# Performance work log

Hardware: AMD Instinct MI355X
Metric: run time of the kernel (lower is better)

The kernel has to match this reference:

```python
import jax, jax.numpy as jnp
import numpy as np

N_NODES = 50000
NEG_SLOPE = 0.2


def setup_inputs() -> dict:
    key = jax.random.key(0)
    k1, k2, k3, k4 = jax.random.split(key, 4)
    N, E, F, H, C = 50000, 800000, 128, 4, 32
    x = jax.random.normal(k1, (N, F), dtype=jnp.float32)
    edge_index = jax.random.randint(k2, (2, E), 0, N, dtype=jnp.int32)
    weight = jax.random.normal(k3, (F, H * C), dtype=jnp.float32) * 0.1  # glorot-ish scale
    att = jax.random.normal(k4, (1, H, 2 * C), dtype=jnp.float32) * 0.1
    bias = jnp.zeros((C,), dtype=jnp.float32)
    return {"x": x, "edge_index": edge_index, "weight": weight, "att": att, "bias": bias}


def reference(x, edge_index, weight, att, bias):
    N = x.shape[0]
    H, C2 = att.shape[1], att.shape[2]
    C = C2 // 2
    # linear projection -> [N, H, C]
    xw = jnp.matmul(x, weight).reshape(N, H, C)
    row, col = edge_index[0], edge_index[1]
    # per-edge attention logits: gather both endpoints, concat along channel
    x_i = xw[row]                     # [E, H, C]
    x_j = xw[col]                     # [E, H, C]
    cat_x = jnp.concatenate([x_i, x_j], axis=-1)      # [E, H, 2C]
    alpha = jnp.sum(cat_x * att, axis=-1)             # [E, H]
    alpha = jnp.where(alpha >= 0, alpha, NEG_SLOPE * alpha)  # leaky_relu
    # segment softmax grouped by row (source index, as in the torch code)
    seg_max = jax.ops.segment_max(alpha, row, num_segments=N)
    seg_max = jnp.where(jnp.isfinite(seg_max), seg_max, 0.0)
    alpha = jnp.exp(alpha - seg_max[row])
    seg_sum = jax.ops.segment_sum(alpha, row, num_segments=N)
    alpha = alpha / (seg_sum[row] + 1e-16)            # [E, H]
    # PyG propagate: message = alpha * x_j where x_j = x[edge_index[0]],
    # aggregated (scatter-add) into target = edge_index[1]
    msg = alpha[..., None] * xw[row]                  # [E, H, C]
    out = jax.ops.segment_sum(msg, col, num_segments=N)  # [N, H, C]
    out = out.mean(axis=1) + bias                     # concat=False -> head mean, + bias
    return out
```

## Files before the change

kernel.cpp:

```cpp
#include <hip/hip_runtime.h>
#include <hip/hip_fp16.h>

#define FDIM 128
#define HEADS 4
#define CD 32
#define BM 64
#define XPAD 68

static __device__ __forceinline__ unsigned short f2bf(float v) {
    unsigned u = __float_as_uint(v);
    u += 0x7FFF + ((u >> 16) & 1);
    return (unsigned short)(u >> 16);
}
static __device__ __forceinline__ float bf2f(unsigned short u) {
    return __uint_as_float(((unsigned)u) << 16);
}

__global__ __launch_bounds__(256) void k_gemm(const float* __restrict__ x,
                                              const float* __restrict__ w,
                                              const float* __restrict__ att,
                                              unsigned short* __restrict__ xwh,
                                              float* __restrict__ a_src,
                                              float* __restrict__ a_dst,
                                              float4* __restrict__ zero_base,
                                              int nz4, int N)
{
    __shared__ float xs[FDIM * XPAD];
    __shared__ float attl[HEADS * 2 * CD];
    int t = threadIdx.x;
    int row0 = blockIdx.x * BM;
    for (int i = blockIdx.x * 256 + t; i < nz4; i += gridDim.x * 256)
        zero_base[i] = make_float4(0.f, 0.f, 0.f, 0.f);
    attl[t] = att[t];
#pragma unroll
    for (int it = 0; it < 8; it++) {
        int i = t + 256 * it;
        int row = i & 63, kq = i >> 6;
        float4 v = make_float4(0.f, 0.f, 0.f, 0.f);
        if (row0 + row < N) v = ((const float4*)x)[(size_t)(row0 + row) * 32 + kq];
        xs[(kq * 4 + 0) * XPAD + row] = v.x;
        xs[(kq * 4 + 1) * XPAD + row] = v.y;
        xs[(kq * 4 + 2) * XPAD + row] = v.z;
        xs[(kq * 4 + 3) * XPAD + row] = v.w;
    }
    __syncthreads();
    int tx = t & 31, ty = t >> 5;
    int c0 = tx * 4, r0 = ty * 8;
    const float4* w4 = (const float4*)w;
    float acc[8][4];
#pragma unroll
    for (int i = 0; i < 8; i++)
#pragma unroll
        for (int j = 0; j < 4; j++) acc[i][j] = 0.f;
#pragma unroll 4
    for (int k = 0; k < FDIM; k++) {
        float4 wv = w4[k * 32 + tx];
        float4 xa = *(const float4*)&xs[k * XPAD + r0];
        float4 xb = *(const float4*)&xs[k * XPAD + r0 + 4];
        float xr[8] = {xa.x, xa.y, xa.z, xa.w, xb.x, xb.y, xb.z, xb.w};
        float wr[4] = {wv.x, wv.y, wv.z, wv.w};
#pragma unroll
        for (int i = 0; i < 8; i++)
#pragma unroll
            for (int j = 0; j < 4; j++) acc[i][j] += xr[i] * wr[j];
    }
    int h0 = c0 >> 5, chb = c0 & 31;
#pragma unroll
    for (int i = 0; i < 8; i++) {
        int r = row0 + r0 + i;
        if (r < N) {
#pragma unroll
            for (int j = 0; j < 4; j++)
                xwh[(size_t)r * FDIM + (chb + j) * 4 + h0] = f2bf(acc[i][j]);
        }
    }
    __syncthreads();
    float* accs = xs;
#pragma unroll
    for (int i = 0; i < 8; i++)
        *(float4*)&accs[(r0 + i) * 132 + c0] =
            make_float4(acc[i][0], acc[i][1], acc[i][2], acc[i][3]);
    __syncthreads();
    int row = t >> 2, h = t & 3;
    const float* ap = &attl[h * 2 * CD];
    const float* xr = &accs[row * 132 + h * CD];
    float s = 0.f, d = 0.f;
#pragma unroll 8
    for (int c = 0; c < CD; c++) { float v = xr[c]; s += v * ap[c]; d += v * ap[CD + c]; }
    int n = row0 + row;
    if (n < N) { a_src[n * 4 + h] = s; a_dst[n * 4 + h] = d; }
}

__global__ __launch_bounds__(256) void k_esum(const int* __restrict__ ei, int E,
                                              const float* __restrict__ a_src,
                                              const float* __restrict__ a_dst,
                                              __half2* __restrict__ seg2,
                                              __half* __restrict__ ealpha)
{
    int gid = blockIdx.x * 256 + threadIdx.x;
    if (gid >= E * HEADS) return;
    int e = gid >> 2, h = gid & 3;
    int r = ei[e], cl = ei[E + e];
    float a = a_src[r * 4 + h] + a_dst[cl * 4 + h];
    a = a >= 0.f ? a : 0.2f * a;
    float ex = __expf(a);
    ealpha[gid] = __float2half(ex);
    float exn = __shfl_down(ex, 1, 64);
    if ((h & 1) == 0)
        unsafeAtomicAdd(&seg2[(size_t)r * 2 + (h >> 1)], __floats2half2_rn(ex, exn));
}

__global__ __launch_bounds__(256) void k_scatter(const int* __restrict__ ei, int E,
                                                 int e0, int e1,
                                                 const __half* __restrict__ ealpha,
                                                 const __half* __restrict__ seg,
                                                 const unsigned short* __restrict__ xwh,
                                                 __half2* __restrict__ out_acc2)
{
    int t = threadIdx.x;
    int le = t >> 4, c2 = t & 15;
    int e = e0 + blockIdx.x * 16 + le;
    if (e >= e1) return;
    int r = ei[e], cl = ei[E + e];
    int lane = t & 63;
    float av = 0.f;
    if (c2 < 4)
        av = 0.25f * __half2float(ealpha[e * 4 + c2]) /
             (__half2float(seg[r * 4 + c2]) + 1e-16f);
    uint4 q = ((const uint4*)(xwh + (size_t)r * FDIM))[c2];
    float a0 = __shfl(av, (lane & 48) + 0, 64);
    float a1 = __shfl(av, (lane & 48) + 1, 64);
    float a2 = __shfl(av, (lane & 48) + 2, 64);
    float a3 = __shfl(av, (lane & 48) + 3, 64);
    float v0 = a0 * bf2f((unsigned short)(q.x & 0xFFFF)) + a1 * bf2f((unsigned short)(q.x >> 16))
             + a2 * bf2f((unsigned short)(q.y & 0xFFFF)) + a3 * bf2f((unsigned short)(q.y >> 16));
    float v1 = a0 * bf2f((unsigned short)(q.z & 0xFFFF)) + a1 * bf2f((unsigned short)(q.z >> 16))
             + a2 * bf2f((unsigned short)(q.w & 0xFFFF)) + a3 * bf2f((unsigned short)(q.w >> 16));
    unsafeAtomicAdd(&out_acc2[(size_t)cl * 16 + c2], __floats2half2_rn(v0, v1));
}

__global__ void k_final(const __half2* __restrict__ out_acc2, const float4* __restrict__ bias,
                        float4* __restrict__ out, int N)
{
    int i = blockIdx.x * 256 + threadIdx.x;
    if (i >= N * 8) return;
    float4 b = bias[i & 7];
    float2 f0 = __half22float2(out_acc2[i * 2]);
    float2 f1 = __half22float2(out_acc2[i * 2 + 1]);
    out[i] = make_float4(f0.x + b.x, f0.y + b.y, f1.x + b.z, f1.y + b.w);
}

extern "C" void kernel_launch(void* const* d_in, const int* in_sizes, int n_in,
                              void* d_out, int out_size, void* d_ws, size_t ws_size,
                              hipStream_t stream)
{
    const float* x    = (const float*)d_in[0];
    const int*   ei   = (const int*)d_in[1];
    const float* w    = (const float*)d_in[2];
    const float* att  = (const float*)d_in[3];
    const float* bias = (const float*)d_in[4];
    float* out = (float*)d_out;
    int N = in_sizes[0] / FDIM;
    int E = in_sizes[1] / 2;

    unsigned short* xwh = (unsigned short*)d_ws;
    float* fws      = (float*)(xwh + (size_t)N * FDIM);
    float* a_src    = fws;
    float* a_dst    = a_src + (size_t)N * HEADS;
    __half* seg     = (__half*)(a_dst + (size_t)N * HEADS);
    __half2* out_acc2 = (__half2*)(seg + (size_t)N * HEADS);
    __half* ealpha  = (__half*)(out_acc2 + (size_t)N * 16);

    int nz4 = (N * 9) / 2;
    int Eh = E / 2;

    k_gemm<<<(N + BM - 1) / BM, 256, 0, stream>>>(x, w, att, xwh, a_src, a_dst,
                                                  (float4*)seg, nz4, N);
    k_esum<<<(E * HEADS + 255) / 256, 256, 0, stream>>>(ei, E, a_src, a_dst,
                                                        (__half2*)seg, ealpha);
    k_scatter<<<(Eh + 15) / 16, 256, 0, stream>>>(ei, E, 0, Eh, ealpha, seg, xwh, out_acc2);
    k_scatter<<<(E - Eh + 15) / 16, 256, 0, stream>>>(ei, E, Eh, E, ealpha, seg, xwh, out_acc2);
    k_final<<<(N * 8 + 255) / 256, 256, 0, stream>>>(out_acc2, (const float4*)bias, (float4*)out, N);
}
```

Measured before the change: 211.9 us.

## Shrink GEMM tile, shuffle-reduce attention logits, vectorize esum per edge, merge scatter

The GEMM block tile is halved to 32 rows, and the attention-logit dot products are now computed from register accumulators with an xor-shuffle reduction. That removes the shared-memory staging and the extra barriers. The edge-sum kernel now uses one thread per edge with float4 loads for all four heads and a packed half store. The two split scatter launches are merged into one. The trade-offs are less reuse per GEMM block and a few extra shuffles.

```diff
diff --git a/kernel.cpp b/kernel.cpp
--- a/kernel.cpp
+++ b/kernel.cpp
@@ -4,8 +4,7 @@
 #define FDIM 128
 #define HEADS 4
 #define CD 32
-#define BM 64
-#define XPAD 68
+#define BM 32
 
 static __device__ __forceinline__ unsigned short f2bf(float v) {
     unsigned u = __float_as_uint(v);
@@ -25,70 +24,75 @@
                                               float4* __restrict__ zero_base,
                                               int nz4, int N)
 {
-    __shared__ float xs[FDIM * XPAD];
-    __shared__ float attl[HEADS * 2 * CD];
+    __shared__ float xs[FDIM * 33];
     int t = threadIdx.x;
     int row0 = blockIdx.x * BM;
     for (int i = blockIdx.x * 256 + t; i < nz4; i += gridDim.x * 256)
         zero_base[i] = make_float4(0.f, 0.f, 0.f, 0.f);
-    attl[t] = att[t];
 #pragma unroll
-    for (int it = 0; it < 8; it++) {
+    for (int it = 0; it < 4; it++) {
         int i = t + 256 * it;
-        int row = i & 63, kq = i >> 6;
+        int row = i >> 5, kq = i & 31;
         float4 v = make_float4(0.f, 0.f, 0.f, 0.f);
         if (row0 + row < N) v = ((const float4*)x)[(size_t)(row0 + row) * 32 + kq];
-        xs[(kq * 4 + 0) * XPAD + row] = v.x;
-        xs[(kq * 4 + 1) * XPAD + row] = v.y;
-        xs[(kq * 4 + 2) * XPAD + row] = v.z;
-        xs[(kq * 4 + 3) * XPAD + row] = v.w;
+        xs[(kq * 4 + 0) * 33 + row] = v.x;
+        xs[(kq * 4 + 1) * 33 + row] = v.y;
+        xs[(kq * 4 + 2) * 33 + row] = v.z;
+        xs[(kq * 4 + 3) * 33 + row] = v.w;
     }
     __syncthreads();
     int tx = t & 31, ty = t >> 5;
-    int c0 = tx * 4, r0 = ty * 8;
+    int c0 = tx * 4, r0 = ty * 4;
     const float4* w4 = (const float4*)w;
-    float acc[8][4];
+    float acc[4][4];
 #pragma unroll
-    for (int i = 0; i < 8; i++)
+    for (int i = 0; i < 4; i++)
 #pragma unroll
         for (int j = 0; j < 4; j++) acc[i][j] = 0.f;
 #pragma unroll 4
     for (int k = 0; k < FDIM; k++) {
         float4 wv = w4[k * 32 + tx];
-        float4 xa = *(const float4*)&xs[k * XPAD + r0];
-        float4 xb = *(const float4*)&xs[k * XPAD + r0 + 4];
-        float xr[8] = {xa.x, xa.y, xa.z, xa.w, xb.x, xb.y, xb.z, xb.w};
+        float4 xa = *(const float4*)&xs[k * 33 + r0];
+        float xr[4] = {xa.x, xa.y, xa.z, xa.w};
         float wr[4] = {wv.x, wv.y, wv.z, wv.w};
 #pragma unroll
-        for (int i = 0; i < 8; i++)
+        for (int i = 0; i < 4; i++)
 #pragma unroll
             for (int j = 0; j < 4; j++) acc[i][j] += xr[i] * wr[j];
     }
-    int h0 = c0 >> 5, chb = c0 & 31;
+    int h = tx >> 3, chb = c0 & 31;
 #pragma unroll
-    for (int i = 0; i < 8; i++) {
+    for (int i = 0; i < 4; i++) {
         int r = row0 + r0 + i;
         if (r < N) {
 #pragma unroll
             for (int j = 0; j < 4; j++)
-                xwh[(size_t)r * FDIM + (chb + j) * 4 + h0] = f2bf(acc[i][j]);
+                xwh[(size_t)r * FDIM + (chb + j) * 4 + h] = f2bf(acc[i][j]);
         }
     }
-    __syncthreads();
-    float* accs = xs;
+    int sub = tx & 7;
+    const float* ap = att + h * 2 * CD + sub * 4;
+    float sv[4], dv[4];
 #pragma unroll
-    for (int i = 0; i < 8; i++)
-        *(float4*)&accs[(r0 + i) * 132 + c0] =
-            make_float4(acc[i][0], acc[i][1], acc[i][2], acc[i][3]);
-    __syncthreads();
-    int row = t >> 2, h = t & 3;
-    const float* ap = &attl[h * 2 * CD];
-    const float* xr = &accs[row * 132 + h * CD];
-    float s = 0.f, d = 0.f;
-#pragma unroll 8
-    for (int c = 0; c < CD; c++) { float v = xr[c]; s += v * ap[c]; d += v * ap[CD + c]; }
-    int n = row0 + row;
-    if (n < N) { a_src[n * 4 + h] = s; a_dst[n * 4 + h] = d; }
+    for (int i = 0; i < 4; i++) {
+        sv[i] = acc[i][0] * ap[0] + acc[i][1] * ap[1] + acc[i][2] * ap[2] + acc[i][3] * ap[3];
+        dv[i] = acc[i][0] * ap[32] + acc[i][1] * ap[33] + acc[i][2] * ap[34] + acc[i][3] * ap[35];
+    }
+#pragma unroll
+    for (int m = 1; m <= 4; m <<= 1) {
+#pragma unroll
+        for (int i = 0; i < 4; i++) {
+            sv[i] += __shfl_xor(sv[i], m, 64);
+            dv[i] += __shfl_xor(dv[i], m, 64);
+        }
+    }
+    if (sub == 0) {
+#pragma unroll
+        for (int i = 0; i < 4; i++) {
+            int n = row0 + r0 + i;
+            if (n < N) { a_src[n * 4 + h] = sv[i]; a_dst[n * 4 + h] = dv[i]; }
+        }
+    }
 }
 
 __global__ __launch_bounds__(256) void k_esum(const int* __restrict__ ei, int E,
@@ -97,21 +101,27 @@
                                               __half2* __restrict__ seg2,
                                               __half* __restrict__ ealpha)
 {
-    int gid = blockIdx.x * 256 + threadIdx.x;
-    if (gid >= E * HEADS) return;
-    int e = gid >> 2, h = gid & 3;
+    int e = blockIdx.x * 256 + threadIdx.x;
+    if (e >= E) return;
     int r = ei[e], cl = ei[E + e];
-    float a = a_src[r * 4 + h] + a_dst[cl * 4 + h];
-    a = a >= 0.f ? a : 0.2f * a;
-    float ex = __expf(a);
-    ealpha[gid] = __float2half(ex);
-    float exn = __shfl_down(ex, 1, 64);
-    if ((h & 1) == 0)
-        unsafeAtomicAdd(&seg2[(size_t)r * 2 + (h >> 1)], __floats2half2_rn(ex, exn));
+    float4 as = *(const float4*)&a_src[r * 4];
+    float4 ad = *(const float4*)&a_dst[cl * 4];
+    float a0 = as.x + ad.x, a1 = as.y + ad.y, a2 = as.z + ad.z, a3 = as.w + ad.w;
+    a0 = a0 >= 0.f ? a0 : 0.2f * a0;
+    a1 = a1 >= 0.f ? a1 : 0.2f * a1;
+    a2 = a2 >= 0.f ? a2 : 0.2f * a2;
+    a3 = a3 >= 0.f ? a3 : 0.2f * a3;
+    __half2 p0 = __floats2half2_rn(__expf(a0), __expf(a1));
+    __half2 p1 = __floats2half2_rn(__expf(a2), __expf(a3));
+    uint2 pkd;
+    pkd.x = *reinterpret_cast<unsigned*>(&p0);
+    pkd.y = *reinterpret_cast<unsigned*>(&p1);
+    ((uint2*)ealpha)[e] = pkd;
+    unsafeAtomicAdd(&seg2[(size_t)r * 2], p0);
+    unsafeAtomicAdd(&seg2[(size_t)r * 2 + 1], p1);
 }
 
 __global__ __launch_bounds__(256) void k_scatter(const int* __restrict__ ei, int E,
-                                                 int e0, int e1,
                                                  const __half* __restrict__ ealpha,
                                                  const __half* __restrict__ seg,
                                                  const unsigned short* __restrict__ xwh,
@@ -119,8 +129,8 @@
 {
     int t = threadIdx.x;
     int le = t >> 4, c2 = t & 15;
-    int e = e0 + blockIdx.x * 16 + le;
-    if (e >= e1) return;
+    int e = blockIdx.x * 16 + le;
+    if (e >= E) return;
     int r = ei[e], cl = ei[E + e];
     int lane = t & 63;
     float av = 0.f;
@@ -172,13 +182,11 @@
     __half* ealpha  = (__half*)(out_acc2 + (size_t)N * 16);
 
     int nz4 = (N * 9) / 2;
-    int Eh = E / 2;
 
     k_gemm<<<(N + BM - 1) / BM, 256, 0, stream>>>(x, w, att, xwh, a_src, a_dst,
                                                   (float4*)seg, nz4, N);
-    k_esum<<<(E * HEADS + 255) / 256, 256, 0, stream>>>(ei, E, a_src, a_dst,
-                                                        (__half2*)seg, ealpha);
-    k_scatter<<<(Eh + 15) / 16, 256, 0, stream>>>(ei, E, 0, Eh, ealpha, seg, xwh, out_acc2);
-    k_scatter<<<(E - Eh + 15) / 16, 256, 0, stream>>>(ei, E, Eh, E, ealpha, seg, xwh, out_acc2);
+    k_esum<<<(E + 255) / 256, 256, 0, stream>>>(ei, E, a_src, a_dst,
+                                                (__half2*)seg, ealpha);
+    k_scatter<<<(E + 15) / 16, 256, 0, stream>>>(ei, E, ealpha, seg, xwh, out_acc2);
     k_final<<<(N * 8 + 255) / 256, 256, 0, stream>>>(out_acc2, (const float4*)bias, (float4*)out, N);
 }
```

Result: slower. 255.1 us (+20.4%).
